# Optimization experiments

Hardware: AMD Instinct MI355X
Metric: run time of the kernel (lower is better)

## Reference

```python
import jax, jax.numpy as jnp
import numpy as np

B, ORDER, N, D, H = 16, 2, 512, 128, 8
DH = D // H
NEG_SLOPE = 0.2


def setup_inputs() -> dict:
    key = jax.random.key(0)
    ks = jax.random.split(key, 8)
    stdv = 1.0 / np.sqrt(DH)

    def u(k, shape):
        return jax.random.uniform(k, shape, jnp.float32, -stdv, stdv)

    x = jax.random.normal(ks[0], (B, ORDER, N, D), jnp.float32)
    A = jax.random.randint(ks[1], (B, ORDER, N, N), 0, 5, jnp.int32)
    # Stacked params for the 2*order GAT modules: axis0 = order, axis1 = (conv1, conv2)
    W = u(ks[2], (ORDER, 2, D, D))            # project.weight
    pb = jnp.zeros((ORDER, 2, D), jnp.float32)  # project.bias (init 0)
    att_src = u(ks[3], (ORDER, 2, H, DH))
    att_dst = u(ks[4], (ORDER, 2, H, DH))
    bias = jnp.zeros((ORDER, 2, D), jnp.float32)  # GAT output bias (init 0)
    return {"x": x, "A": A, "W": W, "pb": pb,
            "att_src": att_src, "att_dst": att_dst, "bias": bias}


def _gat(x, Af, W, pb, a_src, a_dst, b):
    # x: [B,N,D]; Af: [B,N,N] float in {0,1}
    xp = x @ W.T + pb                                  # project
    xh = xp.reshape(B, N, H, DH)                       # [B,N,H,DH]
    s_src = jnp.einsum('bnhd,hd->bnh', xh, a_src)      # [B,N,H]
    s_dst = jnp.einsum('bnhd,hd->bnh', xh, a_dst)
    alpha = s_src[:, :, None, :] + s_dst[:, None, :, :]  # [B,src,dst,H]
    alpha = jnp.where((Af != 1.0)[..., None], 0.0, alpha)
    alpha = jnp.where(alpha >= 0, alpha, NEG_SLOPE * alpha)  # leaky relu
    alpha = jax.nn.softmax(alpha, axis=1)              # softmax over src dim
    out = jnp.einsum('bsdh,bshf->bdhf', alpha, xh).reshape(B, N, D)
    out = out + xp                                     # add_self_loops
    return out + b


def reference(x, A, W, pb, att_src, att_dst, bias):
    A1 = ((A == 2) | (A == 4)).astype(x.dtype)  # [B,ORDER,N,N]
    A2 = ((A == 3) | (A == 4)).astype(x.dtype)
    hs = []
    for i in range(ORDER):
        h1 = _gat(x[:, i], A1[:, i], W[i, 0], pb[i, 0], att_src[i, 0], att_dst[i, 0], bias[i, 0])
        h2 = _gat(x[:, i], A2[:, i], W[i, 1], pb[i, 1], att_src[i, 1], att_dst[i, 1], bias[i, 1])
        hs.append(h1 + h2)
    h = jnp.stack(hs, axis=1)                          # [B,ORDER,N,D]
    out = h + h.mean(axis=1, keepdims=True)
    return out
```

## Files before the change

kernel.cpp:

```cpp
#include <hip/hip_runtime.h>

#define N_ 512
#define D_ 128
#define LOG2E 1.44269504088896f


typedef __attribute__((ext_vector_type(8))) short short8;
typedef __attribute__((ext_vector_type(4))) float floatx4;
typedef __attribute__((ext_vector_type(4))) unsigned int uintx4;
typedef __attribute__((ext_vector_type(2))) _Float16 half2v;
typedef __attribute__((ext_vector_type(8))) _Float16 half8;

#if defined(__has_builtin)
#if __has_builtin(__builtin_amdgcn_exp2f)
#define EXP2F(x) __builtin_amdgcn_exp2f(x)
#else
#define EXP2F(x) exp2f(x)
#endif
#else
#define EXP2F(x) exp2f(x)
#endif

__device__ __forceinline__ unsigned int pkh(float a, float b) {
    auto h = __builtin_amdgcn_cvt_pkrtz(a, b);
    return __builtin_bit_cast(unsigned int, h);
}

__global__ __launch_bounds__(256) void prep_kernel(
    const float* __restrict__ x, const float* __restrict__ W,
    const float* __restrict__ pb, const float* __restrict__ att_src,
    const float* __restrict__ att_dst, const int* __restrict__ A,
    unsigned short* __restrict__ xpt, unsigned int* __restrict__ sgEs,
    unsigned int* __restrict__ sgFs, float2* __restrict__ sgD,
    unsigned int* __restrict__ mgT)
{
    __shared__ _Float16 va_l[8][136];
    __shared__ float c0_l[8];

    const int bid0 = blockIdx.x;
    const int t = threadIdx.x;

    if (bid0 >= 1024) {
        const int bid = bid0 - 1024;
        const int bi = bid >> 4;
        const int rem = bid & 15;
        const int dg = rem >> 2;
        const int jw = rem & 3;
        const int dp = t & 63, q = t >> 6;
        const int dstb = dg * 128 + dp * 2;
        const int sbase = jw * 128 + q * 8;
        const int* Ab = A + (size_t)bi * N_ * N_ + dstb;
        unsigned int a00 = 0, a01 = 0, a10 = 0, a11 = 0;
#pragma unroll
        for (int cp = 0; cp < 4; ++cp) {
#pragma unroll
            for (int i = 0; i < 8; ++i) {
                const int s = sbase + cp * 32 + i;
                const int2 v = *(const int2*)(Ab + (size_t)s * N_);
                const int bitp = cp * 8 + i;
                a00 |= ((0x14u >> v.x) & 1u) << bitp;
                a10 |= ((0x18u >> v.x) & 1u) << bitp;
                a01 |= ((0x14u >> v.y) & 1u) << bitp;
                a11 |= ((0x18u >> v.y) & 1u) << bitp;
            }
        }
        const int i0 = bi * 2;
        mgT[(((size_t)i0 * 4 + q) * 512 + dstb + 0) * 4 + jw] = a00;
        mgT[(((size_t)i0 * 4 + q) * 512 + dstb + 1) * 4 + jw] = a01;
        mgT[(((size_t)(i0 + 1) * 4 + q) * 512 + dstb + 0) * 4 + jw] = a10;
        mgT[(((size_t)(i0 + 1) * 4 + q) * 512 + dstb + 1) * 4 + jw] = a11;
        return;
    }

    const int unit = bid0 >> 1;
    const int half = bid0 & 1;
    const int ntile = unit & 7;
    const int inst  = unit >> 3;
    const int j = inst & 1;
    const int bi = inst >> 1;
    const int ij = (bi & 1) * 2 + j;
    const int wave = t >> 6, L = t & 63, n = L & 15, q = L >> 4;
    const float* wb = W + (size_t)ij * D_ * D_;

    {
        const int c = t >> 5;
        const int k0 = (t & 31) * 4;
        const int hn = half * 4 + (c & 3);
        const float* av = ((c < 4) ? att_src : att_dst) + ij * D_ + hn * 16;
        const float* Wh = wb + (size_t)(hn * 16) * D_ + k0;
        float a0 = 0.f, a1 = 0.f, a2 = 0.f, a3 = 0.f;
#pragma unroll
        for (int dd = 0; dd < 16; ++dd) {
            const float a = av[dd];
            const float4 wv = *(const float4*)(Wh + (size_t)dd * D_);
            a0 += wv.x * a; a1 += wv.y * a; a2 += wv.z * a; a3 += wv.w * a;
        }
        va_l[c][k0 + 0] = (_Float16)(a0 * LOG2E);
        va_l[c][k0 + 1] = (_Float16)(a1 * LOG2E);
        va_l[c][k0 + 2] = (_Float16)(a2 * LOG2E);
        va_l[c][k0 + 3] = (_Float16)(a3 * LOG2E);
        if (t < 8) {
            const int hn2 = half * 4 + (t & 3);
            const float* av2 = ((t < 4) ? att_src : att_dst) + ij * D_ + hn2 * 16;
            const float* pbp = pb + ij * D_ + hn2 * 16;
            float s = 0.f;
#pragma unroll
            for (int dd = 0; dd < 16; ++dd) s += pbp[dd] * av2[dd];
            c0_l[t] = s * LOG2E;
        }
    }

    const int n0w = ntile * 64 + wave * 16;
    const float* xrow = x + ((size_t)bi * N_ + n0w + n) * D_ + q * 8;
    half8 Af[4];
#pragma unroll
    for (int kc = 0; kc < 4; ++kc) {
        const float4 a0 = *(const float4*)(xrow + kc * 32);
        const float4 a1 = *(const float4*)(xrow + kc * 32 + 4);
        uintx4 au;
        au.x = pkh(a0.x, a0.y);
        au.y = pkh(a0.z, a0.w);
        au.z = pkh(a1.x, a1.y);
        au.w = pkh(a1.z, a1.w);
        Af[kc] = __builtin_bit_cast(half8, au);
    }

    __syncthreads();

    floatx4 S = (floatx4){0.f, 0.f, 0.f, 0.f};
    {
        const _Float16* var = &va_l[n & 7][q * 8];
#pragma unroll
        for (int kc = 0; kc < 4; ++kc) {
            const half8 Bs = *(const half8*)(var + kc * 32);
            S = __builtin_amdgcn_mfma_f32_16x16x32_f16(Af[kc], Bs, S, 0, 0, 0);
        }
    }

#pragma unroll
    for (int ft = 0; ft < 4; ++ft) {
        const int head = half * 4 + ft;
        const int fg = head * 16 + n;
        const float* wrow = wb + (size_t)fg * D_ + q * 8;
        floatx4 C = (floatx4){0.f, 0.f, 0.f, 0.f};
#pragma unroll
        for (int kc = 0; kc < 4; ++kc) {
            const float4 b0 = *(const float4*)(wrow + kc * 32);
            const float4 b1 = *(const float4*)(wrow + kc * 32 + 4);
            uintx4 bu;
            bu.x = pkh(b0.x, b0.y);
            bu.y = pkh(b0.z, b0.w);
            bu.z = pkh(b1.x, b1.y);
            bu.w = pkh(b1.z, b1.w);
            C = __builtin_amdgcn_mfma_f32_16x16x32_f16(
                Af[kc], __builtin_bit_cast(half8, bu), C, 0, 0, 0);
        }
        const float pbv = pb[ij * D_ + fg];
        uint2 pk;
        pk.x = pkh(C[0] + pbv, C[1] + pbv);
        pk.y = pkh(C[2] + pbv, C[3] + pbv);
        *(uint2*)&xpt[((size_t)inst * D_ + fg) * N_ + n0w + q * 4] = pk;
    }

    if (n < 8) {
        const float cc = c0_l[n];
        const float v0 = S[0] + cc, v1 = S[1] + cc;
        const float v2 = S[2] + cc, v3 = S[3] + cc;
        if (n < 4) {
            const int head = half * 4 + n;
            const size_t base = ((size_t)inst * 8 + head) * 256 + (n0w >> 1) + q * 2;
            sgEs[base + 0] = pkh(EXP2F(v0), EXP2F(v1));
            sgEs[base + 1] = pkh(EXP2F(v2), EXP2F(v3));
            sgFs[base + 0] = pkh(EXP2F(0.2f * v0), EXP2F(0.2f * v1));
            sgFs[base + 1] = pkh(EXP2F(0.2f * v2), EXP2F(0.2f * v3));
        } else {
            const int head = half * 4 + (n - 4);
            const size_t base = ((size_t)inst * 8 + head) * N_ + n0w + q * 4;
            float2 e0; e0.x = EXP2F(v0); e0.y = EXP2F(0.2f * v0); sgD[base + 0] = e0;
            float2 e1; e1.x = EXP2F(v1); e1.y = EXP2F(0.2f * v1); sgD[base + 1] = e1;
            float2 e2; e2.x = EXP2F(v2); e2.y = EXP2F(0.2f * v2); sgD[base + 2] = e2;
            float2 e3; e3.x = EXP2F(v3); e3.y = EXP2F(0.2f * v3); sgD[base + 3] = e3;
        }
    }
}

__global__ __launch_bounds__(1024, 8) void attn_kernel(
    const unsigned short* __restrict__ xpt,
    const unsigned int* __restrict__ sgEs,
    const unsigned int* __restrict__ sgFs,
    const float2* __restrict__ sgD,
    const unsigned int* __restrict__ mgT,
    const float* __restrict__ bias,
    float* __restrict__ hout)
{
    __shared__ unsigned int smem[16384];

    const int bid = blockIdx.x;
    const int xcd = bid & 7;
    const int idx = bid >> 3;
    const int b   = xcd * 2 + (idx >> 5);
    const int tile = idx & 31;
    const int b4  = b * 4;
    const int d0 = tile * 16;
    const int t = threadIdx.x;
    const int wave = t >> 6, L = t & 63, n = L & 15, q = L >> 4;
    const int io = wave >> 3;
    const int cv = (wave >> 2) & 1;
    const int h0 = (wave & 3) * 2;
    const int il = io * 2 + cv;
    const int inst = b4 + il;
    const int ij = il;

    {
        const uint4* sE = (const uint4*)(sgEs + (size_t)b4 * 2048);
        const uint4* sF = (const uint4*)(sgFs + (size_t)b4 * 2048);
        uint4* dE = (uint4*)smem;
        uint4* dF = (uint4*)(smem + 8192);
        dE[t] = sE[t]; dE[1024 + t] = sE[1024 + t];
        dF[t] = sF[t]; dF[1024 + t] = sF[1024 + t];
    }

    const uint4 mreg = *(const uint4*)(mgT + (((size_t)inst * 4 + q) * 512 + d0 + n) * 4);
    const unsigned int mw_[4] = { mreg.x, mreg.y, mreg.z, mreg.w };

    unsigned int iEd2[2], rd2[2];
#pragma unroll
    for (int hh = 0; hh < 2; ++hh) {
        const float2 ed = sgD[((size_t)inst * 8 + h0 + hh) * N_ + d0 + n];
        const float iEd = 1.0f / ed.x;
        const float rdv = ed.y * iEd;
        iEd2[hh] = pkh(iEd, iEd);
        rd2[hh] = pkh(rdv, rdv);
    }

    __syncthreads();

    const unsigned short* xpi = xpt + (size_t)inst * D_ * N_;
    const unsigned short* bp0 = xpi + (size_t)(h0 * 16 + n) * N_;
    const unsigned short* bp1 = xpi + (size_t)((h0 + 1) * 16 + n) * N_;
    const unsigned int* esw = smem + il * 2048;
    const unsigned int* fsw = smem + 8192 + il * 2048;

    const uintx4 ou = { 0x3C003C00u, 0x3C003C00u, 0x3C003C00u, 0x3C003C00u };
    const half8 onesB = __builtin_bit_cast(half8, ou);

    floatx4 Cacc[2] = { (floatx4){0.f,0.f,0.f,0.f}, (floatx4){0.f,0.f,0.f,0.f} };
    floatx4 Cz[2]   = { (floatx4){0.f,0.f,0.f,0.f}, (floatx4){0.f,0.f,0.f,0.f} };

    uintx4 A0 = *(const uintx4*)(bp0 + q * 8);
    uintx4 A1 = *(const uintx4*)(bp1 + q * 8);
    uintx4 P0 = *(const uintx4*)(bp0 + 32 + q * 8);
    uintx4 P1 = *(const uintx4*)(bp1 + 32 + q * 8);
#pragma unroll
    for (int c = 0; c < 16; ++c) {
        uintx4 F0, F1;
        if (c < 14) {
            F0 = *(const uintx4*)(bp0 + (c + 2) * 32 + q * 8);
            F1 = *(const uintx4*)(bp1 + (c + 2) * 32 + q * 8);
        }
        const unsigned int word = mw_[c >> 2];
        unsigned int sel[4];
#pragma unroll
        for (int p = 0; p < 4; ++p) {
            const int sh = (c & 3) * 8 + 2 * p;
            const unsigned int wb2 = word >> sh;
            sel[p] = ((wb2 & 1u) ? 0x0000FFFFu : 0u) |
                     ((wb2 & 2u) ? 0xFFFF0000u : 0u);
        }
        const int spb = c * 16 + q * 4;
#pragma unroll
        for (int hh = 0; hh < 2; ++hh) {
            const uint4 Ep = *(const uint4*)&esw[(h0 + hh) * 256 + spb];
            const uint4 Fp = *(const uint4*)&fsw[(h0 + hh) * 256 + spb];
            const unsigned int eu[4] = { Ep.x, Ep.y, Ep.z, Ep.w };
            const unsigned int fu[4] = { Fp.x, Fp.y, Fp.z, Fp.w };
            const half2v rdh = __builtin_bit_cast(half2v, rd2[hh]);
            uintx4 au;
            unsigned int wts[4];
#pragma unroll
            for (int p = 0; p < 4; ++p) {
                const half2v e = __builtin_bit_cast(half2v, eu[p]);
                const half2v f = __builtin_bit_cast(half2v, fu[p]);
                const half2v pr = f * rdh;
                const half2v wv = __builtin_elementwise_max(pr, e);
                const unsigned int wvu = __builtin_bit_cast(unsigned int, wv);
                wts[p] = (sel[p] & wvu) | (~sel[p] & iEd2[hh]);
            }
            au.x = wts[0]; au.y = wts[1]; au.z = wts[2]; au.w = wts[3];
            const half8 As = __builtin_bit_cast(half8, au);
            Cacc[hh] = __builtin_amdgcn_mfma_f32_16x16x32_f16(
                As, __builtin_bit_cast(half8, hh ? A1 : A0), Cacc[hh], 0, 0, 0);
            Cz[hh] = __builtin_amdgcn_mfma_f32_16x16x32_f16(
                As, onesB, Cz[hh], 0, 0, 0);
        }
        A0 = P0; A1 = P1;
        P0 = F0; P1 = F1;
    }

    float vals[2][4];
#pragma unroll
    for (int hh = 0; hh < 2; ++hh) {
        const int h = h0 + hh;
        const float bv = bias[ij * D_ + h * 16 + n];
        const uint2 sv = *(const uint2*)(xpi + (size_t)(h * 16 + n) * N_ + d0 + q * 4);
        const half2v s0 = __builtin_bit_cast(half2v, sv.x);
        const half2v s1 = __builtin_bit_cast(half2v, sv.y);
        const float selfv[4] = { (float)s0[0], (float)s0[1],
                                 (float)s1[0], (float)s1[1] };
#pragma unroll
        for (int reg = 0; reg < 4; ++reg) {
            const float Zi = 1.0f / Cz[hh][reg];
            vals[hh][reg] = Cacc[hh][reg] * Zi + selfv[reg] + bv;
        }
    }

    __syncthreads();
    float* out_l = (float*)smem + io * 2112;
    if (cv == 1) {
#pragma unroll
        for (int hh = 0; hh < 2; ++hh)
#pragma unroll
            for (int reg = 0; reg < 4; ++reg)
                out_l[(q * 4 + reg) * 132 + (h0 + hh) * 16 + n] = vals[hh][reg];
    }
    __syncthreads();
    if (cv == 0) {
#pragma unroll
        for (int hh = 0; hh < 2; ++hh)
#pragma unroll
            for (int reg = 0; reg < 4; ++reg) {
                vals[hh][reg] += out_l[(q * 4 + reg) * 132 + (h0 + hh) * 16 + n];
                out_l[(q * 4 + reg) * 132 + (h0 + hh) * 16 + n] = vals[hh][reg];
            }
    }
    __syncthreads();
    if (cv == 0) {
        const float* oth = (const float*)smem + (1 - io) * 2112;
#pragma unroll
        for (int hh = 0; hh < 2; ++hh)
#pragma unroll
            for (int reg = 0; reg < 4; ++reg) {
                const float other = oth[(q * 4 + reg) * 132 + (h0 + hh) * 16 + n];
                hout[((size_t)(b * 2 + io) * N_ + d0 + q * 4 + reg) * D_ +
                     (h0 + hh) * 16 + n] = 1.5f * vals[hh][reg] + 0.5f * other;
            }
    }
}

extern "C" void kernel_launch(void* const* d_in, const int* in_sizes, int n_in,
                              void* d_out, int out_size, void* d_ws, size_t ws_size,
                              hipStream_t stream)
{
    const float* x   = (const float*)d_in[0];
    const int*   A   = (const int*)d_in[1];
    const float* W   = (const float*)d_in[2];
    const float* pb  = (const float*)d_in[3];
    const float* as_ = (const float*)d_in[4];
    const float* ad_ = (const float*)d_in[5];
    const float* bs  = (const float*)d_in[6];

    unsigned short* xpt = (unsigned short*)d_ws;
    unsigned int* sgEs = (unsigned int*)((char*)d_ws + (8u << 20));
    unsigned int* sgFs = (unsigned int*)((char*)d_ws + (8u << 20) + (512u << 10));
    float2* sgD = (float2*)((char*)d_ws + (9u << 20));
    unsigned int* mgT = (unsigned int*)((char*)d_ws + (11u << 20));
    float* h = (float*)d_out;

    prep_kernel<<<1536, 256, 0, stream>>>(x, W, pb, as_, ad_, A, xpt, sgEs, sgFs, sgD, mgT);
    attn_kernel<<<512, 1024, 0, stream>>>(xpt, sgEs, sgFs, sgD, mgT, bs, h);
}
```

Baseline: 146.3 us.

## Process two destination tiles per attention block to reuse source loads

Each attention block now covers two 16-wide destination tiles instead of one, which halves the grid to 256 blocks. The per-block shared-memory staging of E/F tables and the xp B-operand loads are shared across both tiles, so the redundant global and LDS traffic per output is cut. In exchange, register use per thread roughly doubles, the launch-bounds occupancy hint drops from 8 to 4, and the smaller grid may leave some compute units idle on a 256-CU device.

```diff
diff --git a/kernel.cpp b/kernel.cpp
--- a/kernel.cpp
+++ b/kernel.cpp
@@ -184,7 +184,7 @@
     }
 }
 
-__global__ __launch_bounds__(1024, 8) void attn_kernel(
+__global__ __launch_bounds__(1024, 4) void attn_kernel(
     const unsigned short* __restrict__ xpt,
     const unsigned int* __restrict__ sgEs,
     const unsigned int* __restrict__ sgFs,
@@ -198,10 +198,10 @@
     const int bid = blockIdx.x;
     const int xcd = bid & 7;
     const int idx = bid >> 3;
-    const int b   = xcd * 2 + (idx >> 5);
-    const int tile = idx & 31;
+    const int b   = xcd * 2 + (idx >> 4);
+    const int tp  = idx & 15;
+    const int d0a = tp * 32;
     const int b4  = b * 4;
-    const int d0 = tile * 16;
     const int t = threadIdx.x;
     const int wave = t >> 6, L = t & 63, n = L & 15, q = L >> 4;
     const int io = wave >> 3;
@@ -220,17 +220,23 @@
         dF[t] = sF[t]; dF[1024 + t] = sF[1024 + t];
     }
 
-    const uint4 mreg = *(const uint4*)(mgT + (((size_t)inst * 4 + q) * 512 + d0 + n) * 4);
-    const unsigned int mw_[4] = { mreg.x, mreg.y, mreg.z, mreg.w };
-
-    unsigned int iEd2[2], rd2[2];
-#pragma unroll
-    for (int hh = 0; hh < 2; ++hh) {
-        const float2 ed = sgD[((size_t)inst * 8 + h0 + hh) * N_ + d0 + n];
-        const float iEd = 1.0f / ed.x;
-        const float rdv = ed.y * iEd;
-        iEd2[hh] = pkh(iEd, iEd);
-        rd2[hh] = pkh(rdv, rdv);
+    unsigned int mw_[2][4];
+    unsigned int iEd2[2][2], rd2[2][2];
+#pragma unroll
+    for (int tt = 0; tt < 2; ++tt) {
+        const int d0 = d0a + tt * 16;
+        const uint4 mreg =
+            *(const uint4*)(mgT + (((size_t)inst * 4 + q) * 512 + d0 + n) * 4);
+        mw_[tt][0] = mreg.x; mw_[tt][1] = mreg.y;
+        mw_[tt][2] = mreg.z; mw_[tt][3] = mreg.w;
+#pragma unroll
+        for (int hh = 0; hh < 2; ++hh) {
+            const float2 ed = sgD[((size_t)inst * 8 + h0 + hh) * N_ + d0 + n];
+            const float iEd = 1.0f / ed.x;
+            const float rdv = ed.y * iEd;
+            iEd2[tt][hh] = pkh(iEd, iEd);
+            rd2[tt][hh] = pkh(rdv, rdv);
+        }
     }
 
     __syncthreads();
@@ -244,8 +250,10 @@
     const uintx4 ou = { 0x3C003C00u, 0x3C003C00u, 0x3C003C00u, 0x3C003C00u };
     const half8 onesB = __builtin_bit_cast(half8, ou);
 
-    floatx4 Cacc[2] = { (floatx4){0.f,0.f,0.f,0.f}, (floatx4){0.f,0.f,0.f,0.f} };
-    floatx4 Cz[2]   = { (floatx4){0.f,0.f,0.f,0.f}, (floatx4){0.f,0.f,0.f,0.f} };
+    floatx4 Cacc[2][2] = { { (floatx4){0.f,0.f,0.f,0.f}, (floatx4){0.f,0.f,0.f,0.f} },
+                           { (floatx4){0.f,0.f,0.f,0.f}, (floatx4){0.f,0.f,0.f,0.f} } };
+    floatx4 Cz[2][2]   = { { (floatx4){0.f,0.f,0.f,0.f}, (floatx4){0.f,0.f,0.f,0.f} },
+                           { (floatx4){0.f,0.f,0.f,0.f}, (floatx4){0.f,0.f,0.f,0.f} } };
 
     uintx4 A0 = *(const uintx4*)(bp0 + q * 8);
     uintx4 A1 = *(const uintx4*)(bp1 + q * 8);
@@ -258,15 +266,6 @@
             F0 = *(const uintx4*)(bp0 + (c + 2) * 32 + q * 8);
             F1 = *(const uintx4*)(bp1 + (c + 2) * 32 + q * 8);
         }
-        const unsigned int word = mw_[c >> 2];
-        unsigned int sel[4];
-#pragma unroll
-        for (int p = 0; p < 4; ++p) {
-            const int sh = (c & 3) * 8 + 2 * p;
-            const unsigned int wb2 = word >> sh;
-            sel[p] = ((wb2 & 1u) ? 0x0000FFFFu : 0u) |
-                     ((wb2 & 2u) ? 0xFFFF0000u : 0u);
-        }
         const int spb = c * 16 + q * 4;
 #pragma unroll
         for (int hh = 0; hh < 2; ++hh) {
@@ -274,76 +273,108 @@
             const uint4 Fp = *(const uint4*)&fsw[(h0 + hh) * 256 + spb];
             const unsigned int eu[4] = { Ep.x, Ep.y, Ep.z, Ep.w };
             const unsigned int fu[4] = { Fp.x, Fp.y, Fp.z, Fp.w };
-            const half2v rdh = __builtin_bit_cast(half2v, rd2[hh]);
-            uintx4 au;
-            unsigned int wts[4];
-#pragma unroll
-            for (int p = 0; p < 4; ++p) {
-                const half2v e = __builtin_bit_cast(half2v, eu[p]);
-                const half2v f = __builtin_bit_cast(half2v, fu[p]);
-                const half2v pr = f * rdh;
-                const half2v wv = __builtin_elementwise_max(pr, e);
-                const unsigned int wvu = __builtin_bit_cast(unsigned int, wv);
-                wts[p] = (sel[p] & wvu) | (~sel[p] & iEd2[hh]);
+            const half8 Bc = __builtin_bit_cast(half8, hh ? A1 : A0);
+#pragma unroll
+            for (int tt = 0; tt < 2; ++tt) {
+                const half2v rdh = __builtin_bit_cast(half2v, rd2[tt][hh]);
+                const unsigned int word = mw_[tt][c >> 2];
+                uintx4 au;
+                unsigned int wts[4];
+#pragma unroll
+                for (int p = 0; p < 4; ++p) {
+                    const int sh = (c & 3) * 8 + 2 * p;
+                    const unsigned int wb2 = word >> sh;
+                    const unsigned int sel =
+                        ((wb2 & 1u) ? 0x0000FFFFu : 0u) |
+                        ((wb2 & 2u) ? 0xFFFF0000u : 0u);
+                    const half2v e = __builtin_bit_cast(half2v, eu[p]);
+                    const half2v f = __builtin_bit_cast(half2v, fu[p]);
+                    const half2v pr = f * rdh;
+                    const half2v wv = __builtin_elementwise_max(pr, e);
+                    const unsigned int wvu = __builtin_bit_cast(unsigned int, wv);
+                    wts[p] = (sel & wvu) | (~sel & iEd2[tt][hh]);
+                }
+                au.x = wts[0]; au.y = wts[1]; au.z = wts[2]; au.w = wts[3];
+                const half8 As = __builtin_bit_cast(half8, au);
+                Cacc[tt][hh] = __builtin_amdgcn_mfma_f32_16x16x32_f16(
+                    As, Bc, Cacc[tt][hh], 0, 0, 0);
+                Cz[tt][hh] = __builtin_amdgcn_mfma_f32_16x16x32_f16(
+                    As, onesB, Cz[tt][hh], 0, 0, 0);
             }
-            au.x = wts[0]; au.y = wts[1]; au.z = wts[2]; au.w = wts[3];
-            const half8 As = __builtin_bit_cast(half8, au);
-            Cacc[hh] = __builtin_amdgcn_mfma_f32_16x16x32_f16(
-                As, __builtin_bit_cast(half8, hh ? A1 : A0), Cacc[hh], 0, 0, 0);
-            Cz[hh] = __builtin_amdgcn_mfma_f32_16x16x32_f16(
-                As, onesB, Cz[hh], 0, 0, 0);
         }
         A0 = P0; A1 = P1;
         P0 = F0; P1 = F1;
     }
 
-    float vals[2][4];
-#pragma unroll
-    for (int hh = 0; hh < 2; ++hh) {
-        const int h = h0 + hh;
-        const float bv = bias[ij * D_ + h * 16 + n];
-        const uint2 sv = *(const uint2*)(xpi + (size_t)(h * 16 + n) * N_ + d0 + q * 4);
-        const half2v s0 = __builtin_bit_cast(half2v, sv.x);
-        const half2v s1 = __builtin_bit_cast(half2v, sv.y);
-        const float selfv[4] = { (float)s0[0], (float)s0[1],
-                                 (float)s1[0], (float)s1[1] };
-#pragma unroll
-        for (int reg = 0; reg < 4; ++reg) {
-            const float Zi = 1.0f / Cz[hh][reg];
-            vals[hh][reg] = Cacc[hh][reg] * Zi + selfv[reg] + bv;
+    float vals[2][2][4];
+#pragma unroll
+    for (int tt = 0; tt < 2; ++tt) {
+        const int d0 = d0a + tt * 16;
+#pragma unroll
+        for (int hh = 0; hh < 2; ++hh) {
+            const int h = h0 + hh;
+            const float bv = bias[ij * D_ + h * 16 + n];
+            const uint2 sv =
+                *(const uint2*)(xpi + (size_t)(h * 16 + n) * N_ + d0 + q * 4);
+            const half2v s0 = __builtin_bit_cast(half2v, sv.x);
+            const half2v s1 = __builtin_bit_cast(half2v, sv.y);
+            const float selfv[4] = { (float)s0[0], (float)s0[1],
+                                     (float)s1[0], (float)s1[1] };
+#pragma unroll
+            for (int reg = 0; reg < 4; ++reg) {
+                const float Zi = 1.0f / Cz[tt][hh][reg];
+                vals[tt][hh][reg] = Cacc[tt][hh][reg] * Zi + selfv[reg] + bv;
+            }
         }
     }
 
     __syncthreads();
-    float* out_l = (float*)smem + io * 2112;
+    float* smf = (float*)smem;
     if (cv == 1) {
 #pragma unroll
-        for (int hh = 0; hh < 2; ++hh)
-#pragma unroll
-            for (int reg = 0; reg < 4; ++reg)
-                out_l[(q * 4 + reg) * 132 + (h0 + hh) * 16 + n] = vals[hh][reg];
+        for (int tt = 0; tt < 2; ++tt) {
+            float* out_l = smf + (tt * 2 + io) * 2112;
+#pragma unroll
+            for (int hh = 0; hh < 2; ++hh)
+#pragma unroll
+                for (int reg = 0; reg < 4; ++reg)
+                    out_l[(q * 4 + reg) * 132 + (h0 + hh) * 16 + n] =
+                        vals[tt][hh][reg];
+        }
     }
     __syncthreads();
     if (cv == 0) {
 #pragma unroll
-        for (int hh = 0; hh < 2; ++hh)
-#pragma unroll
-            for (int reg = 0; reg < 4; ++reg) {
-                vals[hh][reg] += out_l[(q * 4 + reg) * 132 + (h0 + hh) * 16 + n];
-                out_l[(q * 4 + reg) * 132 + (h0 + hh) * 16 + n] = vals[hh][reg];
-            }
+        for (int tt = 0; tt < 2; ++tt) {
+            float* out_l = smf + (tt * 2 + io) * 2112;
+#pragma unroll
+            for (int hh = 0; hh < 2; ++hh)
+#pragma unroll
+                for (int reg = 0; reg < 4; ++reg) {
+                    vals[tt][hh][reg] +=
+                        out_l[(q * 4 + reg) * 132 + (h0 + hh) * 16 + n];
+                    out_l[(q * 4 + reg) * 132 + (h0 + hh) * 16 + n] =
+                        vals[tt][hh][reg];
+                }
+        }
     }
     __syncthreads();
     if (cv == 0) {
-        const float* oth = (const float*)smem + (1 - io) * 2112;
-#pragma unroll
-        for (int hh = 0; hh < 2; ++hh)
-#pragma unroll
-            for (int reg = 0; reg < 4; ++reg) {
-                const float other = oth[(q * 4 + reg) * 132 + (h0 + hh) * 16 + n];
-                hout[((size_t)(b * 2 + io) * N_ + d0 + q * 4 + reg) * D_ +
-                     (h0 + hh) * 16 + n] = 1.5f * vals[hh][reg] + 0.5f * other;
-            }
+#pragma unroll
+        for (int tt = 0; tt < 2; ++tt) {
+            const int d0 = d0a + tt * 16;
+            const float* oth = smf + (tt * 2 + (1 - io)) * 2112;
+#pragma unroll
+            for (int hh = 0; hh < 2; ++hh)
+#pragma unroll
+                for (int reg = 0; reg < 4; ++reg) {
+                    const float other =
+                        oth[(q * 4 + reg) * 132 + (h0 + hh) * 16 + n];
+                    hout[((size_t)(b * 2 + io) * N_ + d0 + q * 4 + reg) * D_ +
+                         (h0 + hh) * 16 + n] =
+                        1.5f * vals[tt][hh][reg] + 0.5f * other;
+                }
+        }
     }
 }
 
@@ -367,5 +398,5 @@
     float* h = (float*)d_out;
 
     prep_kernel<<<1536, 256, 0, stream>>>(x, W, pb, as_, ad_, A, xpt, sgEs, sgFs, sgD, mgT);
-    attn_kernel<<<512, 1024, 0, stream>>>(xpt, sgEs, sgFs, sgD, mgT, bs, h);
+    attn_kernel<<<256, 1024, 0, stream>>>(xpt, sgEs, sgFs, sgD, mgT, bs, h);
 }
```

Result: faster. 135.8 us (-7.2%).
